# Kernel optimization log

Measured on AMD Instinct MI355X. Metric: run time of the kernel, lower is better.

Reference implementation:

```python
import jax, jax.numpy as jnp
import numpy as np
import math

B, N, D = 8, 4096, 1024
H = 8          # num_heads
NC = 2         # n_classes


def setup_inputs() -> dict:
    key = jax.random.key(0)
    ks = jax.random.split(key, 12)
    s = 1.0 / math.sqrt(D)
    return {
        "inputs": jax.random.normal(ks[0], (B, N, D), jnp.float32),
        # enc: Linear(D, 1) + Sigmoid
        "W_enc": jax.random.normal(ks[1], (1, D), jnp.float32) * s,
        "b_enc": jnp.zeros((1,), jnp.float32),
        "cls_token": jax.random.normal(ks[2], (1, 1, D), jnp.float32) * s,
        # depthwise Conv2d(D, D, 3, padding=1, groups=D)
        "conv_w": jax.random.normal(ks[3], (D, 1, 3, 3), jnp.float32) * 0.1,
        "conv_b": jnp.zeros((D,), jnp.float32),
        # MAB projections (torch Linear weight layout [out, in])
        "Wq": jax.random.normal(ks[4], (D, D), jnp.float32) * s,
        "bq": jnp.zeros((D,), jnp.float32),
        "Wk": jax.random.normal(ks[5], (D, D), jnp.float32) * s,
        "bk": jnp.zeros((D,), jnp.float32),
        "Wv": jax.random.normal(ks[6], (D, D), jnp.float32) * s,
        "bv": jnp.zeros((D,), jnp.float32),
        "Wo": jax.random.normal(ks[7], (D, D), jnp.float32) * s,
        "bo": jnp.zeros((D,), jnp.float32),
        # final classifier Linear(D, NC)
        "Wfc": jax.random.normal(ks[8], (NC, D), jnp.float32) * s,
        "bfc": jnp.zeros((NC,), jnp.float32),
    }


def reference(inputs, W_enc, b_enc, cls_token, conv_w, conv_b,
              Wq, bq, Wk, bk, Wv, bv, Wo, bo, Wfc, bfc):
    b, n, d = inputs.shape
    # ---- recalib(option='max', k=1): top-1 instance per bag as query ----
    a1 = jax.nn.sigmoid(inputs @ W_enc.T + b_enc)[..., 0]            # [B, N]
    idx = jnp.argmax(a1, axis=1)                                      # [B]
    Q = jnp.take_along_axis(inputs, idx[:, None, None], axis=1)       # [B, 1, D]
    # ---- shift_feature ----
    inputs = jax.nn.relu(inputs - Q)
    # ---- pad to square grid, prepend cls token ----
    _H = int(np.ceil(np.sqrt(n)))
    add = _H * _H - n
    x = jnp.concatenate([inputs, inputs[:, :add, :]], axis=1)         # [B, _H*_H, D]
    cls = jnp.broadcast_to(cls_token, (b, 1, d))
    x = jnp.concatenate([cls, x], axis=1)                             # [B, S, D]
    cls_tok, feat = x[:, 0], x[:, 1:]
    # ---- depthwise conv residual on the 2D grid ----
    cnn = feat.transpose(0, 2, 1).reshape(b, d, _H, _H)               # [B, C, H, W]
    conv = jax.lax.conv_general_dilated(
        cnn, conv_w, window_strides=(1, 1), padding='SAME',
        dimension_numbers=('NCHW', 'OIHW', 'NCHW'),
        feature_group_count=d) + conv_b[None, :, None, None]
    cnn = conv + cnn
    xf = cnn.reshape(b, d, _H * _H).transpose(0, 2, 1)
    x = jnp.concatenate([cls_tok[:, None, :], xf], axis=1)            # [B, S, D]
    # ---- MAB(Q, x): manual multi-head attention ----
    Qp = Q @ Wq.T + bq                                                # [B, 1, D]
    K = x @ Wk.T + bk                                                 # [B, S, D]
    V = x @ Wv.T + bv
    dh = d // H
    qh = Qp.reshape(b, 1, H, dh).transpose(0, 2, 1, 3)                # [B, H, 1, dh]
    kh = K.reshape(b, -1, H, dh).transpose(0, 2, 1, 3)                # [B, H, S, dh]
    vh = V.reshape(b, -1, H, dh).transpose(0, 2, 1, 3)
    # NOTE: original scales by sqrt(dim_V), not sqrt(d_head)
    logits = jnp.einsum('bhqd,bhkd->bhqk', qh, kh) / jnp.asarray(math.sqrt(d), jnp.float32)
    A = jax.nn.softmax(logits, axis=-1)
    oh = qh + jnp.einsum('bhqk,bhkd->bhqd', A, vh)                    # residual inside heads
    O = oh.transpose(0, 2, 1, 3).reshape(b, 1, d)                     # [B, 1, D]
    O = O + jax.nn.relu(O @ Wo.T + bo)
    bag = O[:, 0]                                                     # [B, D]
    out = bag @ Wfc.T + bfc                                           # [B, NC]
    return out
```

## Files before the change

kernel.cpp:

```cpp
#include <hip/hip_runtime.h>
#include <hip/hip_bf16.h>


#define NTOK 4096
#define DD 1024

#define FO_ARG 0
#define FO_S1  16
#define FO_CWT 4160
#define FO_QP  13376
#define FO_W   21568
#define FO_MS  87232
#define FO_YP  95424
#define FO_Y   4289728
#define FO_O1  4355264
#define FO_O2  4363456

#define LSTRIDE 101

__global__ void k_init(const float* __restrict__ convw, float* __restrict__ cwT) {
  int gid = blockIdx.x * 256 + threadIdx.x;
  if (gid < 9216) {
    int d = gid / 9, p = gid - d * 9;
    cwT[p * DD + d] = convw[gid];
  }
}

__global__ void k_argmax1(const float* __restrict__ inp, const float* __restrict__ Wenc,
                          const float* __restrict__ benc, unsigned long long* __restrict__ s1buf) {
  __shared__ unsigned long long lb[4];
  int wave = threadIdx.x >> 6, lane = threadIdx.x & 63;
  int b = blockIdx.x >> 8;
  int r0 = ((blockIdx.x & 255) << 4) + (wave << 2);
  const float4* base = (const float4*)(inp + ((size_t)b * NTOK + r0) * DD);
  const float4* wp = (const float4*)Wenc;
  float s0 = 0.f, s1 = 0.f, s2 = 0.f, s3 = 0.f;
#pragma unroll
  for (int k = 0; k < 4; ++k) {
    int off = lane + (k << 6);
    float4 w4 = wp[off];
    float4 a0 = base[off];
    float4 a1 = base[256 + off];
    float4 a2 = base[512 + off];
    float4 a3 = base[768 + off];
    s0 = fmaf(w4.x, a0.x, s0); s0 = fmaf(w4.y, a0.y, s0); s0 = fmaf(w4.z, a0.z, s0); s0 = fmaf(w4.w, a0.w, s0);
    s1 = fmaf(w4.x, a1.x, s1); s1 = fmaf(w4.y, a1.y, s1); s1 = fmaf(w4.z, a1.z, s1); s1 = fmaf(w4.w, a1.w, s1);
    s2 = fmaf(w4.x, a2.x, s2); s2 = fmaf(w4.y, a2.y, s2); s2 = fmaf(w4.z, a2.z, s2); s2 = fmaf(w4.w, a2.w, s2);
    s3 = fmaf(w4.x, a3.x, s3); s3 = fmaf(w4.y, a3.y, s3); s3 = fmaf(w4.z, a3.z, s3); s3 = fmaf(w4.w, a3.w, s3);
  }
#pragma unroll
  for (int mk = 32; mk >= 1; mk >>= 1) {
    s0 += __shfl_xor(s0, mk); s1 += __shfl_xor(s1, mk);
    s2 += __shfl_xor(s2, mk); s3 += __shfl_xor(s3, mk);
  }
  if (lane == 0) {
    float be = benc[0];
    float v[4] = {s0 + be, s1 + be, s2 + be, s3 + be};
    unsigned long long bst = 0ull;
#pragma unroll
    for (int i = 0; i < 4; ++i) {
      unsigned u = __float_as_uint(v[i]);
      u = (u & 0x80000000u) ? ~u : (u | 0x80000000u);
      unsigned long long p = ((unsigned long long)u << 32) |
                             (unsigned long long)(0xFFFFFFFFu - (unsigned)(r0 + i));
      bst = bst > p ? bst : p;
    }
    lb[wave] = bst;
  }
  __syncthreads();
  if (threadIdx.x == 0) {
    unsigned long long m = lb[0];
#pragma unroll
    for (int i = 1; i < 4; ++i) m = m > lb[i] ? m : lb[i];
    s1buf[blockIdx.x] = m;
  }
}

__global__ void k_argmax2(const unsigned long long* __restrict__ s1buf,
                          unsigned long long* __restrict__ argbest) {
  __shared__ unsigned long long red[256];
  int tid = threadIdx.x, b = blockIdx.x;
  red[tid] = s1buf[b * 256 + tid];
  __syncthreads();
  for (int s = 128; s > 0; s >>= 1) {
    if (tid < s) { unsigned long long o = red[tid + s]; if (o > red[tid]) red[tid] = o; }
    __syncthreads();
  }
  if (tid == 0) argbest[b] = red[0];
}

__global__ void k_qp(const float* __restrict__ inp, const float* __restrict__ Wq,
                     const float* __restrict__ bq, const unsigned long long* __restrict__ argbest,
                     float* __restrict__ Qp) {
  int wave = threadIdx.x >> 6, lane = threadIdx.x & 63;
  int b = blockIdx.x >> 8;
  int i = ((blockIdx.x & 255) << 2) + wave;
  unsigned idx = 0xFFFFFFFFu - (unsigned)(argbest[b] & 0xFFFFFFFFull);
  const float4* qr = (const float4*)(inp + ((size_t)b * NTOK + idx) * DD);
  const float4* wr = (const float4*)(Wq + (size_t)i * DD);
  float s = 0.f;
#pragma unroll
  for (int k = 0; k < 4; ++k) {
    float4 a = wr[lane + (k << 6)], x = qr[lane + (k << 6)];
    s = fmaf(a.x, x.x, s); s = fmaf(a.y, x.y, s);
    s = fmaf(a.z, x.z, s); s = fmaf(a.w, x.w, s);
  }
  for (int m = 32; m > 0; m >>= 1) s += __shfl_xor(s, m);
  if (lane == 0) Qp[b * DD + i] = s + bq[i];
}

__global__ void k_w(const float* __restrict__ Wk, const float* __restrict__ Qp,
                    float* __restrict__ wbuf) {
  __shared__ float qs[1024];
  __shared__ float sred[2048];
  const int tid = threadIdx.x;
  const int h = blockIdx.x >> 5, jb = blockIdx.x & 31;
  {
    int b = tid >> 5, i4 = tid & 31;
    ((float4*)qs)[b * 32 + i4] = ((const float4*)Qp)[b * 256 + (h << 5) + i4];
  }
  __syncthreads();
  const int jl = tid & 31, ig = tid >> 5;
  const float* wkp = Wk + (size_t)((h << 7) + (ig << 4)) * DD + (jb << 5) + jl;
  float acc[8];
#pragma unroll
  for (int b = 0; b < 8; ++b) acc[b] = 0.f;
#pragma unroll
  for (int ii = 0; ii < 16; ++ii) {
    float wv = wkp[(size_t)ii * DD];
    int i = (ig << 4) + ii;
#pragma unroll
    for (int b = 0; b < 8; ++b) acc[b] = fmaf(qs[(b << 7) + i], wv, acc[b]);
  }
#pragma unroll
  for (int b = 0; b < 8; ++b) sred[ig * 256 + (b << 5) + jl] = acc[b];
  __syncthreads();
  {
    int b = tid >> 5, j2 = tid & 31;
    float s = 0.f;
#pragma unroll
    for (int g = 0; g < 8; ++g) s += sred[g * 256 + (b << 5) + j2];
    wbuf[(size_t)((b << 3) + h) * DD + (jb << 5) + j2] = s;
  }
}

__global__ __launch_bounds__(512, 4) void k_fused(
    const float* __restrict__ inp, const float* __restrict__ convb,
    const float* __restrict__ cwT, const float* __restrict__ wbuf,
    const unsigned long long* __restrict__ argbest,
    float2* __restrict__ msbuf, float* __restrict__ ypart) {
  __shared__ float4 sred4[32 * LSTRIDE];
  __shared__ float atile[512];
  const int tid = threadIdx.x, bx = blockIdx.x;
  const int b = bx >> 6, tile = bx & 63;
  const int R0 = (tile >> 3) << 3, C0 = (tile & 7) << 3;
  const unsigned idxq = 0xFFFFFFFFu - (unsigned)(argbest[b] & 0xFFFFFFFFull);
  const float* inpb = inp + (size_t)b * NTOK * DD;
  const float* qrow = inpb + (size_t)idxq * DD;
  const int gg = tid & 31, ts = tid >> 5;
  const int jg = tid >> 5, rq = (tid >> 3) & 3, ca = tid & 7;
  const int r0a = rq << 1;

  float acc[2][8];
#pragma unroll
  for (int i = 0; i < 2; ++i)
#pragma unroll
    for (int h = 0; h < 8; ++h) acc[i][h] = 0.f;

  for (int cidx = 0; cidx < 8; ++cidx) {
    const int jc = cidx << 7;
    __syncthreads();
    {
      const int js = jc + (gg << 2);
      float4 qv = *(const float4*)(qrow + js);
      for (int t = ts; t < 100; t += 16) {
        int tr = t / 10, tc = t - tr * 10;
        int gr = R0 - 1 + tr, gc = C0 - 1 + tc;
        float4 v = make_float4(0.f, 0.f, 0.f, 0.f);
        if (gr >= 0 && gr < 64 && gc >= 0 && gc < 64) {
          float4 rv = *(const float4*)(inpb + (size_t)((gr << 6) + gc) * DD + js);
          v.x = fmaxf(rv.x - qv.x, 0.f); v.y = fmaxf(rv.y - qv.y, 0.f);
          v.z = fmaxf(rv.z - qv.z, 0.f); v.w = fmaxf(rv.w - qv.w, 0.f);
        }
        sred4[gg * LSTRIDE + t] = v;
      }
    }
    __syncthreads();
#pragma unroll
    for (int sub = 0; sub < 2; ++sub) {
      const int g = (sub << 4) + jg;
      const int j4 = jc + (g << 2);
      float4 cwr[9];
#pragma unroll
      for (int p = 0; p < 9; ++p) cwr[p] = *(const float4*)(cwT + p * DD + j4);
      float4 cb4 = *(const float4*)(convb + j4);
      const float4* fb = sred4 + g * LSTRIDE;
      float4 x0 = cb4, x1 = cb4;
      {
        float4 rw[4][3];
#pragma unroll
        for (int rr = 0; rr < 4; ++rr)
#pragma unroll
          for (int dc = 0; dc < 3; ++dc)
            rw[rr][dc] = fb[(r0a + rr) * 10 + ca + dc];
#pragma unroll
        for (int dr = 0; dr < 3; ++dr)
#pragma unroll
          for (int dc = 0; dc < 3; ++dc) {
            float4 w = cwr[dr * 3 + dc];
            float4 f0 = rw[dr][dc], f1 = rw[dr + 1][dc];
            x0.x = fmaf(w.x, f0.x, x0.x); x0.y = fmaf(w.y, f0.y, x0.y);
            x0.z = fmaf(w.z, f0.z, x0.z); x0.w = fmaf(w.w, f0.w, x0.w);
            x1.x = fmaf(w.x, f1.x, x1.x); x1.y = fmaf(w.y, f1.y, x1.y);
            x1.z = fmaf(w.z, f1.z, x1.z); x1.w = fmaf(w.w, f1.w, x1.w);
          }
        x0.x += rw[1][1].x; x0.y += rw[1][1].y; x0.z += rw[1][1].z; x0.w += rw[1][1].w;
        x1.x += rw[2][1].x; x1.y += rw[2][1].y; x1.z += rw[2][1].z; x1.w += rw[2][1].w;
      }
#pragma unroll
      for (int h = 0; h < 8; ++h) {
        float4 whv = *(const float4*)(wbuf + (size_t)(b * 8 + h) * DD + j4);
        float a0 = acc[0][h], a1 = acc[1][h];
        a0 = fmaf(whv.x, x0.x, a0); a0 = fmaf(whv.y, x0.y, a0);
        a0 = fmaf(whv.z, x0.z, a0); a0 = fmaf(whv.w, x0.w, a0);
        a1 = fmaf(whv.x, x1.x, a1); a1 = fmaf(whv.y, x1.y, a1);
        a1 = fmaf(whv.z, x1.z, a1); a1 = fmaf(whv.w, x1.w, a1);
        acc[0][h] = a0; acc[1][h] = a1;
      }
    }
  }
  __syncthreads();
  float* red = (float*)sred4;
#pragma unroll
  for (int it = 0; it < 2; ++it)
#pragma unroll
    for (int h = 0; h < 8; ++h)
      red[jg * 512 + ((r0a + it) * 8 + ca) * 8 + h] = acc[it][h];
  __syncthreads();
  {
    int o = tid;
    float s = 0.f;
#pragma unroll
    for (int g = 0; g < 16; ++g) s += red[g * 512 + o];
    int h = o & 7, tok = o >> 3;
    atile[h * 64 + tok] = s * 0.03125f;
  }
  __syncthreads();
  if (tid < 256) {
    int hh = tid >> 5, sl = tid & 31;
    float l1 = atile[hh * 64 + sl], l2 = atile[hh * 64 + 32 + sl];
    float mx = fmaxf(l1, l2);
#pragma unroll
    for (int mk = 16; mk >= 1; mk >>= 1) mx = fmaxf(mx, __shfl_xor(mx, mk));
    float e1 = __expf(l1 - mx), e2 = __expf(l2 - mx);
    float Ssum = e1 + e2;
#pragma unroll
    for (int mk = 16; mk >= 1; mk >>= 1) Ssum += __shfl_xor(Ssum, mk);
    atile[hh * 64 + sl] = e1; atile[hh * 64 + 32 + sl] = e2;
    if (sl == 0) msbuf[(b * 8 + hh) * 64 + tile] = make_float2(mx, Ssum);
  }
  const int gB = tid >> 4, rh = (tid >> 3) & 1, cB = tid & 7;
  const int rbase = rh << 2;
  for (int cidx = 0; cidx < 8; ++cidx) {
    const int jc = cidx << 7;
    __syncthreads();
    {
      const int js = jc + (gg << 2);
      float4 qv = *(const float4*)(qrow + js);
      for (int t = ts; t < 100; t += 16) {
        int tr = t / 10, tc = t - tr * 10;
        int gr = R0 - 1 + tr, gc = C0 - 1 + tc;
        float4 v = make_float4(0.f, 0.f, 0.f, 0.f);
        if (gr >= 0 && gr < 64 && gc >= 0 && gc < 64) {
          float4 rv = *(const float4*)(inpb + (size_t)((gr << 6) + gc) * DD + js);
          v.x = fmaxf(rv.x - qv.x, 0.f); v.y = fmaxf(rv.y - qv.y, 0.f);
          v.z = fmaxf(rv.z - qv.z, 0.f); v.w = fmaxf(rv.w - qv.w, 0.f);
        }
        sred4[gg * LSTRIDE + t] = v;
      }
    }
    __syncthreads();
    const int j4 = jc + (gB << 2);
    float4 cwr[9];
#pragma unroll
    for (int p = 0; p < 9; ++p) cwr[p] = *(const float4*)(cwT + p * DD + j4);
    float4 cb4 = *(const float4*)(convb + j4);
    const float4* fb = sred4 + gB * LSTRIDE;
    float4 y4[8];
#pragma unroll
    for (int h = 0; h < 8; ++h) y4[h] = make_float4(0.f, 0.f, 0.f, 0.f);
    float4 w0[3], w1[3], w2[3];
#pragma unroll
    for (int dc = 0; dc < 3; ++dc) {
      w0[dc] = fb[rbase * 10 + cB + dc];
      w1[dc] = fb[(rbase + 1) * 10 + cB + dc];
    }
#pragma unroll
    for (int k = 0; k < 4; ++k) {
#pragma unroll
      for (int dc = 0; dc < 3; ++dc) w2[dc] = fb[(rbase + k + 2) * 10 + cB + dc];
      float4 x4 = cb4;
#pragma unroll
      for (int dc = 0; dc < 3; ++dc) {
        float4 wa = cwr[dc], wb = cwr[3 + dc], wc = cwr[6 + dc];
        x4.x = fmaf(wa.x, w0[dc].x, x4.x); x4.y = fmaf(wa.y, w0[dc].y, x4.y);
        x4.z = fmaf(wa.z, w0[dc].z, x4.z); x4.w = fmaf(wa.w, w0[dc].w, x4.w);
        x4.x = fmaf(wb.x, w1[dc].x, x4.x); x4.y = fmaf(wb.y, w1[dc].y, x4.y);
        x4.z = fmaf(wb.z, w1[dc].z, x4.z); x4.w = fmaf(wb.w, w1[dc].w, x4.w);
        x4.x = fmaf(wc.x, w2[dc].x, x4.x); x4.y = fmaf(wc.y, w2[dc].y, x4.y);
        x4.z = fmaf(wc.z, w2[dc].z, x4.z); x4.w = fmaf(wc.w, w2[dc].w, x4.w);
      }
      x4.x += w1[1].x; x4.y += w1[1].y; x4.z += w1[1].z; x4.w += w1[1].w;
      int tok = ((rbase + k) << 3) + cB;
#pragma unroll
      for (int h = 0; h < 8; ++h) {
        float a = atile[h * 64 + tok];
        y4[h].x = fmaf(a, x4.x, y4[h].x); y4[h].y = fmaf(a, x4.y, y4[h].y);
        y4[h].z = fmaf(a, x4.z, y4[h].z); y4[h].w = fmaf(a, x4.w, y4[h].w);
      }
#pragma unroll
      for (int dc = 0; dc < 3; ++dc) { w0[dc] = w1[dc]; w1[dc] = w2[dc]; }
    }
#pragma unroll
    for (int h = 0; h < 8; ++h)
#pragma unroll
      for (int mk = 8; mk >= 1; mk >>= 1) {
        y4[h].x += __shfl_xor(y4[h].x, mk);
        y4[h].y += __shfl_xor(y4[h].y, mk);
        y4[h].z += __shfl_xor(y4[h].z, mk);
        y4[h].w += __shfl_xor(y4[h].w, mk);
      }
    if ((tid & 15) == 0) {
#pragma unroll
      for (int h = 0; h < 8; ++h)
        *(float4*)(ypart + ((size_t)(b * 8 + h) * 64 + tile) * DD + j4) = y4[h];
    }
  }
}

__global__ void k_comb(const float2* __restrict__ msbuf, const float* __restrict__ wbuf,
                       const float* __restrict__ cls, const float* __restrict__ ypart,
                       float* __restrict__ ybuf) {
  __shared__ float redl[256];
  __shared__ float wgt[64];
  __shared__ float wclss;
  __shared__ float4 sacc[256];
  int tid = threadIdx.x;
  int bh = blockIdx.x >> 3, cs = blockIdx.x & 7;
  {
    float4 a = ((const float4*)(wbuf + (size_t)bh * DD))[tid];
    float4 c = ((const float4*)cls)[tid];
    redl[tid] = a.x * c.x + a.y * c.y + a.z * c.z + a.w * c.w;
  }
  __syncthreads();
  for (int s = 128; s > 0; s >>= 1) { if (tid < s) redl[tid] += redl[tid + s]; __syncthreads(); }
  float l0 = redl[0] * 0.03125f;
  if (tid < 64) {
    float2 ms = msbuf[bh * 64 + tid];
    float m = ms.x, S = ms.y;
    float M = m;
#pragma unroll
    for (int mk = 32; mk >= 1; mk >>= 1) M = fmaxf(M, __shfl_xor(M, mk));
    M = fmaxf(M, l0);
    float w = __expf(m - M);
    float z = S * w;
#pragma unroll
    for (int mk = 32; mk >= 1; mk >>= 1) z += __shfl_xor(z, mk);
    float ec = __expf(l0 - M);
    float Z = z + ec;
    wgt[tid] = w / Z;
    if (tid == 0) wclss = ec / Z;
  }
  __syncthreads();
  int ch4 = (cs << 5) + (tid & 31);
  int tg = tid >> 5;
  const float* yp = ypart + (size_t)bh * 64 * DD + (ch4 << 2);
  float4 acc = make_float4(0.f, 0.f, 0.f, 0.f);
#pragma unroll
  for (int tt = 0; tt < 8; ++tt) {
    int t = tg * 8 + tt;
    float w = wgt[t];
    float4 v = *(const float4*)(yp + (size_t)t * DD);
    acc.x = fmaf(w, v.x, acc.x); acc.y = fmaf(w, v.y, acc.y);
    acc.z = fmaf(w, v.z, acc.z); acc.w = fmaf(w, v.w, acc.w);
  }
  sacc[tg * 32 + (tid & 31)] = acc;
  __syncthreads();
  if (tid < 32) {
    int c4 = (cs << 5) + tid;
    float4 s = sacc[tid];
#pragma unroll
    for (int g = 1; g < 8; ++g) {
      float4 v = sacc[g * 32 + tid];
      s.x += v.x; s.y += v.y; s.z += v.z; s.w += v.w;
    }
    float wc = wclss;
    float4 cv = *(const float4*)(cls + (c4 << 2));
    s.x = fmaf(wc, cv.x, s.x); s.y = fmaf(wc, cv.y, s.y);
    s.z = fmaf(wc, cv.z, s.z); s.w = fmaf(wc, cv.w, s.w);
    *(float4*)(ybuf + (size_t)bh * DD + (c4 << 2)) = s;
  }
}

__global__ void k_o1(const float* __restrict__ Wv, const float* __restrict__ bv,
                     const float* __restrict__ Qp, const float* __restrict__ ybuf,
                     float* __restrict__ O1) {
  int wave = threadIdx.x >> 6, lane = threadIdx.x & 63;
  int b = blockIdx.x >> 8;
  int i = ((blockIdx.x & 255) << 2) + wave;
  int h = i >> 7;
  const float4* wr = (const float4*)(Wv + (size_t)i * DD);
  const float4* yr = (const float4*)(ybuf + (size_t)(b * 8 + h) * DD);
  float s = 0.f;
#pragma unroll
  for (int k = 0; k < 4; ++k) {
    float4 a = wr[lane + (k << 6)], x = yr[lane + (k << 6)];
    s = fmaf(a.x, x.x, s); s = fmaf(a.y, x.y, s);
    s = fmaf(a.z, x.z, s); s = fmaf(a.w, x.w, s);
  }
  for (int m = 32; m > 0; m >>= 1) s += __shfl_xor(s, m);
  if (lane == 0) O1[b * DD + i] = Qp[b * DD + i] + bv[i] + s;
}

__global__ void k_o2(const float* __restrict__ Wo, const float* __restrict__ bo,
                     const float* __restrict__ O1, float* __restrict__ O2) {
  int wave = threadIdx.x >> 6, lane = threadIdx.x & 63;
  int b = blockIdx.x >> 8;
  int i = ((blockIdx.x & 255) << 2) + wave;
  const float4* wr = (const float4*)(Wo + (size_t)i * DD);
  const float4* xr = (const float4*)(O1 + (size_t)b * DD);
  float s = 0.f;
#pragma unroll
  for (int k = 0; k < 4; ++k) {
    float4 a = wr[lane + (k << 6)], x = xr[lane + (k << 6)];
    s = fmaf(a.x, x.x, s); s = fmaf(a.y, x.y, s);
    s = fmaf(a.z, x.z, s); s = fmaf(a.w, x.w, s);
  }
  for (int m = 32; m > 0; m >>= 1) s += __shfl_xor(s, m);
  if (lane == 0) O2[b * DD + i] = O1[b * DD + i] + fmaxf(s + bo[i], 0.f);
}

__global__ void k_out(const float* __restrict__ Wfc, const float* __restrict__ bfc,
                      const float* __restrict__ O2, float* __restrict__ out) {
  int wave = threadIdx.x >> 6, lane = threadIdx.x & 63;
  for (int p = wave; p < 16; p += 4) {
    int b = p >> 1, cc = p & 1;
    const float4* o = (const float4*)(O2 + (size_t)b * DD);
    const float4* wr = (const float4*)(Wfc + (size_t)cc * DD);
    float s = 0.f;
#pragma unroll
    for (int k = 0; k < 4; ++k) {
      float4 a = o[lane + (k << 6)], x = wr[lane + (k << 6)];
      s = fmaf(a.x, x.x, s); s = fmaf(a.y, x.y, s);
      s = fmaf(a.z, x.z, s); s = fmaf(a.w, x.w, s);
    }
    for (int m = 32; m > 0; m >>= 1) s += __shfl_xor(s, m);
    if (lane == 0) out[p] = s + bfc[cc];
  }
}

extern "C" void kernel_launch(void* const* d_in, const int* in_sizes, int n_in,
                              void* d_out, int out_size, void* d_ws, size_t ws_size,
                              hipStream_t stream) {
  const float* inp   = (const float*)d_in[0];
  const float* Wenc  = (const float*)d_in[1];
  const float* benc  = (const float*)d_in[2];
  const float* cls   = (const float*)d_in[3];
  const float* convw = (const float*)d_in[4];
  const float* convb = (const float*)d_in[5];
  const float* Wq    = (const float*)d_in[6];
  const float* bq    = (const float*)d_in[7];
  const float* Wk    = (const float*)d_in[8];
  const float* bv    = (const float*)d_in[11];
  const float* Wv    = (const float*)d_in[10];
  const float* Wo    = (const float*)d_in[12];
  const float* bo    = (const float*)d_in[13];
  const float* Wfc   = (const float*)d_in[14];
  const float* bfc   = (const float*)d_in[15];
  float* out = (float*)d_out;
  float* W = (float*)d_ws;
  unsigned long long* argbest = (unsigned long long*)(W + FO_ARG);
  unsigned long long* s1buf   = (unsigned long long*)(W + FO_S1);
  float* cwT   = W + FO_CWT;
  float* Qp    = W + FO_QP;
  float* wbuf  = W + FO_W;
  float2* msbuf = (float2*)(W + FO_MS);
  float* ypart = W + FO_YP;
  float* ybuf  = W + FO_Y;
  float* O1    = W + FO_O1;
  float* O2    = W + FO_O2;

  hipLaunchKernelGGL(k_init,    dim3(36),   dim3(256), 0, stream, convw, cwT);
  hipLaunchKernelGGL(k_argmax1, dim3(2048), dim3(256), 0, stream, inp, Wenc, benc, s1buf);
  hipLaunchKernelGGL(k_argmax2, dim3(8),    dim3(256), 0, stream, s1buf, argbest);
  hipLaunchKernelGGL(k_qp,      dim3(2048), dim3(256), 0, stream, inp, Wq, bq, argbest, Qp);
  hipLaunchKernelGGL(k_w,       dim3(256),  dim3(256), 0, stream, Wk, Qp, wbuf);
  hipLaunchKernelGGL(k_fused,   dim3(512),  dim3(512), 0, stream, inp, convb, cwT, wbuf, argbest, msbuf, ypart);
  hipLaunchKernelGGL(k_comb,    dim3(512),  dim3(256), 0, stream, msbuf, wbuf, cls, ypart, ybuf);
  hipLaunchKernelGGL(k_o1,      dim3(2048), dim3(256), 0, stream, Wv, bv, Qp, ybuf, O1);
  hipLaunchKernelGGL(k_o2,      dim3(2048), dim3(256), 0, stream, Wo, bo, O1, O2);
  hipLaunchKernelGGL(k_out,     dim3(1),    dim3(256), 0, stream, Wfc, bfc, O2, out);
}
```

Baseline: 387.3 us.

## Split fused conv-attention kernel into channel-parallel logits, softmax and accumulate kernels

The single fused kernel ran 512 blocks, and each block looped over 8 channel chunks in two passes. It is replaced by three kernels. k_logits computes per-chunk partial logits over 4096 blocks. k_sm reduces those partials across chunks and does the tile-local softmax. k_yacc recomputes the conv and accumulates the weighted values, also over 4096 blocks with one chunk each. The goal is to fill the GPU far better than 512 large blocks could. The cost is two extra launches and an 8 MB partial-logit buffer round trip, stored in the ypart region. The per-block halo is still loaded twice per tile, as before.

```diff
diff --git a/kernel.cpp b/kernel.cpp
--- a/kernel.cpp
+++ b/kernel.cpp
@@ -15,6 +15,7 @@
 #define FO_Y   4289728
 #define FO_O1  4355264
 #define FO_O2  4363456
+#define FO_AW  4371648
 
 #define LSTRIDE 101
 
@@ -144,15 +145,14 @@
   }
 }
 
-__global__ __launch_bounds__(512, 4) void k_fused(
+__global__ __launch_bounds__(512, 6) void k_logits(
     const float* __restrict__ inp, const float* __restrict__ convb,
     const float* __restrict__ cwT, const float* __restrict__ wbuf,
     const unsigned long long* __restrict__ argbest,
-    float2* __restrict__ msbuf, float* __restrict__ ypart) {
+    float* __restrict__ plog) {
   __shared__ float4 sred4[32 * LSTRIDE];
-  __shared__ float atile[512];
   const int tid = threadIdx.x, bx = blockIdx.x;
-  const int b = bx >> 6, tile = bx & 63;
+  const int b = bx >> 9, tile = (bx >> 3) & 63, cidx = bx & 7;
   const int R0 = (tile >> 3) << 3, C0 = (tile & 7) << 3;
   const unsigned idxq = 0xFFFFFFFFu - (unsigned)(argbest[b] & 0xFFFFFFFFull);
   const float* inpb = inp + (size_t)b * NTOK * DD;
@@ -160,6 +160,7 @@
   const int gg = tid & 31, ts = tid >> 5;
   const int jg = tid >> 5, rq = (tid >> 3) & 3, ca = tid & 7;
   const int r0a = rq << 1;
+  const int jc = cidx << 7;
 
   float acc[2][8];
 #pragma unroll
@@ -167,66 +168,62 @@
 #pragma unroll
     for (int h = 0; h < 8; ++h) acc[i][h] = 0.f;
 
-  for (int cidx = 0; cidx < 8; ++cidx) {
-    const int jc = cidx << 7;
-    __syncthreads();
+  {
+    const int js = jc + (gg << 2);
+    float4 qv = *(const float4*)(qrow + js);
+    for (int t = ts; t < 100; t += 16) {
+      int tr = t / 10, tc = t - tr * 10;
+      int gr = R0 - 1 + tr, gc = C0 - 1 + tc;
+      float4 v = make_float4(0.f, 0.f, 0.f, 0.f);
+      if (gr >= 0 && gr < 64 && gc >= 0 && gc < 64) {
+        float4 rv = *(const float4*)(inpb + (size_t)((gr << 6) + gc) * DD + js);
+        v.x = fmaxf(rv.x - qv.x, 0.f); v.y = fmaxf(rv.y - qv.y, 0.f);
+        v.z = fmaxf(rv.z - qv.z, 0.f); v.w = fmaxf(rv.w - qv.w, 0.f);
+      }
+      sred4[gg * LSTRIDE + t] = v;
+    }
+  }
+  __syncthreads();
+#pragma unroll
+  for (int sub = 0; sub < 2; ++sub) {
+    const int g = (sub << 4) + jg;
+    const int j4 = jc + (g << 2);
+    float4 cwr[9];
+#pragma unroll
+    for (int p = 0; p < 9; ++p) cwr[p] = *(const float4*)(cwT + p * DD + j4);
+    float4 cb4 = *(const float4*)(convb + j4);
+    const float4* fb = sred4 + g * LSTRIDE;
+    float4 x0 = cb4, x1 = cb4;
     {
-      const int js = jc + (gg << 2);
-      float4 qv = *(const float4*)(qrow + js);
-      for (int t = ts; t < 100; t += 16) {
-        int tr = t / 10, tc = t - tr * 10;
-        int gr = R0 - 1 + tr, gc = C0 - 1 + tc;
-        float4 v = make_float4(0.f, 0.f, 0.f, 0.f);
-        if (gr >= 0 && gr < 64 && gc >= 0 && gc < 64) {
-          float4 rv = *(const float4*)(inpb + (size_t)((gr << 6) + gc) * DD + js);
-          v.x = fmaxf(rv.x - qv.x, 0.f); v.y = fmaxf(rv.y - qv.y, 0.f);
-          v.z = fmaxf(rv.z - qv.z, 0.f); v.w = fmaxf(rv.w - qv.w, 0.f);
+      float4 rw[4][3];
+#pragma unroll
+      for (int rr = 0; rr < 4; ++rr)
+#pragma unroll
+        for (int dc = 0; dc < 3; ++dc)
+          rw[rr][dc] = fb[(r0a + rr) * 10 + ca + dc];
+#pragma unroll
+      for (int dr = 0; dr < 3; ++dr)
+#pragma unroll
+        for (int dc = 0; dc < 3; ++dc) {
+          float4 w = cwr[dr * 3 + dc];
+          float4 f0 = rw[dr][dc], f1 = rw[dr + 1][dc];
+          x0.x = fmaf(w.x, f0.x, x0.x); x0.y = fmaf(w.y, f0.y, x0.y);
+          x0.z = fmaf(w.z, f0.z, x0.z); x0.w = fmaf(w.w, f0.w, x0.w);
+          x1.x = fmaf(w.x, f1.x, x1.x); x1.y = fmaf(w.y, f1.y, x1.y);
+          x1.z = fmaf(w.z, f1.z, x1.z); x1.w = fmaf(w.w, f1.w, x1.w);
         }
-        sred4[gg * LSTRIDE + t] = v;
-      }
-    }
-    __syncthreads();
-#pragma unroll
-    for (int sub = 0; sub < 2; ++sub) {
-      const int g = (sub << 4) + jg;
-      const int j4 = jc + (g << 2);
-      float4 cwr[9];
-#pragma unroll
-      for (int p = 0; p < 9; ++p) cwr[p] = *(const float4*)(cwT + p * DD + j4);
-      float4 cb4 = *(const float4*)(convb + j4);
-      const float4* fb = sred4 + g * LSTRIDE;
-      float4 x0 = cb4, x1 = cb4;
-      {
-        float4 rw[4][3];
-#pragma unroll
-        for (int rr = 0; rr < 4; ++rr)
-#pragma unroll
-          for (int dc = 0; dc < 3; ++dc)
-            rw[rr][dc] = fb[(r0a + rr) * 10 + ca + dc];
-#pragma unroll
-        for (int dr = 0; dr < 3; ++dr)
-#pragma unroll
-          for (int dc = 0; dc < 3; ++dc) {
-            float4 w = cwr[dr * 3 + dc];
-            float4 f0 = rw[dr][dc], f1 = rw[dr + 1][dc];
-            x0.x = fmaf(w.x, f0.x, x0.x); x0.y = fmaf(w.y, f0.y, x0.y);
-            x0.z = fmaf(w.z, f0.z, x0.z); x0.w = fmaf(w.w, f0.w, x0.w);
-            x1.x = fmaf(w.x, f1.x, x1.x); x1.y = fmaf(w.y, f1.y, x1.y);
-            x1.z = fmaf(w.z, f1.z, x1.z); x1.w = fmaf(w.w, f1.w, x1.w);
-          }
-        x0.x += rw[1][1].x; x0.y += rw[1][1].y; x0.z += rw[1][1].z; x0.w += rw[1][1].w;
-        x1.x += rw[2][1].x; x1.y += rw[2][1].y; x1.z += rw[2][1].z; x1.w += rw[2][1].w;
-      }
-#pragma unroll
-      for (int h = 0; h < 8; ++h) {
-        float4 whv = *(const float4*)(wbuf + (size_t)(b * 8 + h) * DD + j4);
-        float a0 = acc[0][h], a1 = acc[1][h];
-        a0 = fmaf(whv.x, x0.x, a0); a0 = fmaf(whv.y, x0.y, a0);
-        a0 = fmaf(whv.z, x0.z, a0); a0 = fmaf(whv.w, x0.w, a0);
-        a1 = fmaf(whv.x, x1.x, a1); a1 = fmaf(whv.y, x1.y, a1);
-        a1 = fmaf(whv.z, x1.z, a1); a1 = fmaf(whv.w, x1.w, a1);
-        acc[0][h] = a0; acc[1][h] = a1;
-      }
+      x0.x += rw[1][1].x; x0.y += rw[1][1].y; x0.z += rw[1][1].z; x0.w += rw[1][1].w;
+      x1.x += rw[2][1].x; x1.y += rw[2][1].y; x1.z += rw[2][1].z; x1.w += rw[2][1].w;
+    }
+#pragma unroll
+    for (int h = 0; h < 8; ++h) {
+      float4 whv = *(const float4*)(wbuf + (size_t)(b * 8 + h) * DD + j4);
+      float a0 = acc[0][h], a1 = acc[1][h];
+      a0 = fmaf(whv.x, x0.x, a0); a0 = fmaf(whv.y, x0.y, a0);
+      a0 = fmaf(whv.z, x0.z, a0); a0 = fmaf(whv.w, x0.w, a0);
+      a1 = fmaf(whv.x, x1.x, a1); a1 = fmaf(whv.y, x1.y, a1);
+      a1 = fmaf(whv.z, x1.z, a1); a1 = fmaf(whv.w, x1.w, a1);
+      acc[0][h] = a0; acc[1][h] = a1;
     }
   }
   __syncthreads();
@@ -238,103 +235,137 @@
       red[jg * 512 + ((r0a + it) * 8 + ca) * 8 + h] = acc[it][h];
   __syncthreads();
   {
-    int o = tid;
     float s = 0.f;
 #pragma unroll
-    for (int g = 0; g < 16; ++g) s += red[g * 512 + o];
-    int h = o & 7, tok = o >> 3;
-    atile[h * 64 + tok] = s * 0.03125f;
-  }
-  __syncthreads();
-  if (tid < 256) {
-    int hh = tid >> 5, sl = tid & 31;
-    float l1 = atile[hh * 64 + sl], l2 = atile[hh * 64 + 32 + sl];
-    float mx = fmaxf(l1, l2);
-#pragma unroll
-    for (int mk = 16; mk >= 1; mk >>= 1) mx = fmaxf(mx, __shfl_xor(mx, mk));
-    float e1 = __expf(l1 - mx), e2 = __expf(l2 - mx);
-    float Ssum = e1 + e2;
-#pragma unroll
-    for (int mk = 16; mk >= 1; mk >>= 1) Ssum += __shfl_xor(Ssum, mk);
-    atile[hh * 64 + sl] = e1; atile[hh * 64 + 32 + sl] = e2;
-    if (sl == 0) msbuf[(b * 8 + hh) * 64 + tile] = make_float2(mx, Ssum);
-  }
+    for (int g = 0; g < 16; ++g) s += red[g * 512 + tid];
+    plog[(size_t)bx * 512 + tid] = s;
+  }
+}
+
+__global__ void k_sm(const float* __restrict__ plog, float* __restrict__ aw,
+                     float2* __restrict__ msbuf) {
+  __shared__ float atile[512];
+  const int tid = threadIdx.x, bt = blockIdx.x;
+  const float* pp = plog + (size_t)bt * 8 * 512;
+  float s0 = 0.f, s1 = 0.f;
+#pragma unroll
+  for (int c = 0; c < 8; ++c) {
+    s0 += pp[c * 512 + tid];
+    s1 += pp[c * 512 + 256 + tid];
+  }
+  {
+    int o = tid, h = o & 7, tok = o >> 3;
+    atile[h * 64 + tok] = s0 * 0.03125f;
+    o = tid + 256; h = o & 7; tok = o >> 3;
+    atile[h * 64 + tok] = s1 * 0.03125f;
+  }
+  __syncthreads();
+  const int hh = tid >> 5, sl = tid & 31;
+  float l1 = atile[hh * 64 + sl], l2 = atile[hh * 64 + 32 + sl];
+  float mx = fmaxf(l1, l2);
+#pragma unroll
+  for (int mk = 16; mk >= 1; mk >>= 1) mx = fmaxf(mx, __shfl_xor(mx, mk));
+  float e1 = __expf(l1 - mx), e2 = __expf(l2 - mx);
+  float Ssum = e1 + e2;
+#pragma unroll
+  for (int mk = 16; mk >= 1; mk >>= 1) Ssum += __shfl_xor(Ssum, mk);
+  aw[(size_t)bt * 512 + hh * 64 + sl] = e1;
+  aw[(size_t)bt * 512 + hh * 64 + 32 + sl] = e2;
+  if (sl == 0) {
+    int b = bt >> 6, tile = bt & 63;
+    msbuf[((b << 3) + hh) * 64 + tile] = make_float2(mx, Ssum);
+  }
+}
+
+__global__ __launch_bounds__(512, 6) void k_yacc(
+    const float* __restrict__ inp, const float* __restrict__ convb,
+    const float* __restrict__ cwT, const float* __restrict__ aw,
+    const unsigned long long* __restrict__ argbest,
+    float* __restrict__ ypart) {
+  __shared__ float4 sred4[32 * LSTRIDE];
+  __shared__ float atile[512];
+  const int tid = threadIdx.x, bx = blockIdx.x;
+  const int b = bx >> 9, tile = (bx >> 3) & 63, cidx = bx & 7;
+  const int R0 = (tile >> 3) << 3, C0 = (tile & 7) << 3;
+  const unsigned idxq = 0xFFFFFFFFu - (unsigned)(argbest[b] & 0xFFFFFFFFull);
+  const float* inpb = inp + (size_t)b * NTOK * DD;
+  const float* qrow = inpb + (size_t)idxq * DD;
+  const int gg = tid & 31, ts = tid >> 5;
+  const int jc = cidx << 7;
+
+  atile[tid] = aw[(size_t)((b << 6) + tile) * 512 + tid];
+  {
+    const int js = jc + (gg << 2);
+    float4 qv = *(const float4*)(qrow + js);
+    for (int t = ts; t < 100; t += 16) {
+      int tr = t / 10, tc = t - tr * 10;
+      int gr = R0 - 1 + tr, gc = C0 - 1 + tc;
+      float4 v = make_float4(0.f, 0.f, 0.f, 0.f);
+      if (gr >= 0 && gr < 64 && gc >= 0 && gc < 64) {
+        float4 rv = *(const float4*)(inpb + (size_t)((gr << 6) + gc) * DD + js);
+        v.x = fmaxf(rv.x - qv.x, 0.f); v.y = fmaxf(rv.y - qv.y, 0.f);
+        v.z = fmaxf(rv.z - qv.z, 0.f); v.w = fmaxf(rv.w - qv.w, 0.f);
+      }
+      sred4[gg * LSTRIDE + t] = v;
+    }
+  }
+  __syncthreads();
   const int gB = tid >> 4, rh = (tid >> 3) & 1, cB = tid & 7;
   const int rbase = rh << 2;
-  for (int cidx = 0; cidx < 8; ++cidx) {
-    const int jc = cidx << 7;
-    __syncthreads();
-    {
-      const int js = jc + (gg << 2);
-      float4 qv = *(const float4*)(qrow + js);
-      for (int t = ts; t < 100; t += 16) {
-        int tr = t / 10, tc = t - tr * 10;
-        int gr = R0 - 1 + tr, gc = C0 - 1 + tc;
-        float4 v = make_float4(0.f, 0.f, 0.f, 0.f);
-        if (gr >= 0 && gr < 64 && gc >= 0 && gc < 64) {
-          float4 rv = *(const float4*)(inpb + (size_t)((gr << 6) + gc) * DD + js);
-          v.x = fmaxf(rv.x - qv.x, 0.f); v.y = fmaxf(rv.y - qv.y, 0.f);
-          v.z = fmaxf(rv.z - qv.z, 0.f); v.w = fmaxf(rv.w - qv.w, 0.f);
-        }
-        sred4[gg * LSTRIDE + t] = v;
-      }
-    }
-    __syncthreads();
-    const int j4 = jc + (gB << 2);
-    float4 cwr[9];
-#pragma unroll
-    for (int p = 0; p < 9; ++p) cwr[p] = *(const float4*)(cwT + p * DD + j4);
-    float4 cb4 = *(const float4*)(convb + j4);
-    const float4* fb = sred4 + gB * LSTRIDE;
-    float4 y4[8];
-#pragma unroll
-    for (int h = 0; h < 8; ++h) y4[h] = make_float4(0.f, 0.f, 0.f, 0.f);
-    float4 w0[3], w1[3], w2[3];
+  const int j4 = jc + (gB << 2);
+  float4 cwr[9];
+#pragma unroll
+  for (int p = 0; p < 9; ++p) cwr[p] = *(const float4*)(cwT + p * DD + j4);
+  float4 cb4 = *(const float4*)(convb + j4);
+  const float4* fb = sred4 + gB * LSTRIDE;
+  float4 y4[8];
+#pragma unroll
+  for (int h = 0; h < 8; ++h) y4[h] = make_float4(0.f, 0.f, 0.f, 0.f);
+  float4 w0[3], w1[3], w2[3];
+#pragma unroll
+  for (int dc = 0; dc < 3; ++dc) {
+    w0[dc] = fb[rbase * 10 + cB + dc];
+    w1[dc] = fb[(rbase + 1) * 10 + cB + dc];
+  }
+#pragma unroll
+  for (int k = 0; k < 4; ++k) {
+#pragma unroll
+    for (int dc = 0; dc < 3; ++dc) w2[dc] = fb[(rbase + k + 2) * 10 + cB + dc];
+    float4 x4 = cb4;
 #pragma unroll
     for (int dc = 0; dc < 3; ++dc) {
-      w0[dc] = fb[rbase * 10 + cB + dc];
-      w1[dc] = fb[(rbase + 1) * 10 + cB + dc];
-    }
-#pragma unroll
-    for (int k = 0; k < 4; ++k) {
-#pragma unroll
-      for (int dc = 0; dc < 3; ++dc) w2[dc] = fb[(rbase + k + 2) * 10 + cB + dc];
-      float4 x4 = cb4;
-#pragma unroll
-      for (int dc = 0; dc < 3; ++dc) {
-        float4 wa = cwr[dc], wb = cwr[3 + dc], wc = cwr[6 + dc];
-        x4.x = fmaf(wa.x, w0[dc].x, x4.x); x4.y = fmaf(wa.y, w0[dc].y, x4.y);
-        x4.z = fmaf(wa.z, w0[dc].z, x4.z); x4.w = fmaf(wa.w, w0[dc].w, x4.w);
-        x4.x = fmaf(wb.x, w1[dc].x, x4.x); x4.y = fmaf(wb.y, w1[dc].y, x4.y);
-        x4.z = fmaf(wb.z, w1[dc].z, x4.z); x4.w = fmaf(wb.w, w1[dc].w, x4.w);
-        x4.x = fmaf(wc.x, w2[dc].x, x4.x); x4.y = fmaf(wc.y, w2[dc].y, x4.y);
-        x4.z = fmaf(wc.z, w2[dc].z, x4.z); x4.w = fmaf(wc.w, w2[dc].w, x4.w);
-      }
-      x4.x += w1[1].x; x4.y += w1[1].y; x4.z += w1[1].z; x4.w += w1[1].w;
-      int tok = ((rbase + k) << 3) + cB;
-#pragma unroll
-      for (int h = 0; h < 8; ++h) {
-        float a = atile[h * 64 + tok];
-        y4[h].x = fmaf(a, x4.x, y4[h].x); y4[h].y = fmaf(a, x4.y, y4[h].y);
-        y4[h].z = fmaf(a, x4.z, y4[h].z); y4[h].w = fmaf(a, x4.w, y4[h].w);
-      }
-#pragma unroll
-      for (int dc = 0; dc < 3; ++dc) { w0[dc] = w1[dc]; w1[dc] = w2[dc]; }
-    }
+      float4 wa = cwr[dc], wb = cwr[3 + dc], wc = cwr[6 + dc];
+      x4.x = fmaf(wa.x, w0[dc].x, x4.x); x4.y = fmaf(wa.y, w0[dc].y, x4.y);
+      x4.z = fmaf(wa.z, w0[dc].z, x4.z); x4.w = fmaf(wa.w, w0[dc].w, x4.w);
+      x4.x = fmaf(wb.x, w1[dc].x, x4.x); x4.y = fmaf(wb.y, w1[dc].y, x4.y);
+      x4.z = fmaf(wb.z, w1[dc].z, x4.z); x4.w = fmaf(wb.w, w1[dc].w, x4.w);
+      x4.x = fmaf(wc.x, w2[dc].x, x4.x); x4.y = fmaf(wc.y, w2[dc].y, x4.y);
+      x4.z = fmaf(wc.z, w2[dc].z, x4.z); x4.w = fmaf(wc.w, w2[dc].w, x4.w);
+    }
+    x4.x += w1[1].x; x4.y += w1[1].y; x4.z += w1[1].z; x4.w += w1[1].w;
+    int tok = ((rbase + k) << 3) + cB;
+#pragma unroll
+    for (int h = 0; h < 8; ++h) {
+      float a = atile[h * 64 + tok];
+      y4[h].x = fmaf(a, x4.x, y4[h].x); y4[h].y = fmaf(a, x4.y, y4[h].y);
+      y4[h].z = fmaf(a, x4.z, y4[h].z); y4[h].w = fmaf(a, x4.w, y4[h].w);
+    }
+#pragma unroll
+    for (int dc = 0; dc < 3; ++dc) { w0[dc] = w1[dc]; w1[dc] = w2[dc]; }
+  }
+#pragma unroll
+  for (int h = 0; h < 8; ++h)
+#pragma unroll
+    for (int mk = 8; mk >= 1; mk >>= 1) {
+      y4[h].x += __shfl_xor(y4[h].x, mk);
+      y4[h].y += __shfl_xor(y4[h].y, mk);
+      y4[h].z += __shfl_xor(y4[h].z, mk);
+      y4[h].w += __shfl_xor(y4[h].w, mk);
+    }
+  if ((tid & 15) == 0) {
 #pragma unroll
     for (int h = 0; h < 8; ++h)
-#pragma unroll
-      for (int mk = 8; mk >= 1; mk >>= 1) {
-        y4[h].x += __shfl_xor(y4[h].x, mk);
-        y4[h].y += __shfl_xor(y4[h].y, mk);
-        y4[h].z += __shfl_xor(y4[h].z, mk);
-        y4[h].w += __shfl_xor(y4[h].w, mk);
-      }
-    if ((tid & 15) == 0) {
-#pragma unroll
-      for (int h = 0; h < 8; ++h)
-        *(float4*)(ypart + ((size_t)(b * 8 + h) * 64 + tile) * DD + j4) = y4[h];
-    }
+      *(float4*)(ypart + ((size_t)(b * 8 + h) * 64 + tile) * DD + j4) = y4[h];
   }
 }
 
@@ -486,6 +517,8 @@
   float* wbuf  = W + FO_W;
   float2* msbuf = (float2*)(W + FO_MS);
   float* ypart = W + FO_YP;
+  float* plog  = W + FO_YP;
+  float* aw    = W + FO_AW;
   float* ybuf  = W + FO_Y;
   float* O1    = W + FO_O1;
   float* O2    = W + FO_O2;
@@ -495,7 +528,9 @@
   hipLaunchKernelGGL(k_argmax2, dim3(8),    dim3(256), 0, stream, s1buf, argbest);
   hipLaunchKernelGGL(k_qp,      dim3(2048), dim3(256), 0, stream, inp, Wq, bq, argbest, Qp);
   hipLaunchKernelGGL(k_w,       dim3(256),  dim3(256), 0, stream, Wk, Qp, wbuf);
-  hipLaunchKernelGGL(k_fused,   dim3(512),  dim3(512), 0, stream, inp, convb, cwT, wbuf, argbest, msbuf, ypart);
+  hipLaunchKernelGGL(k_logits,  dim3(4096), dim3(512), 0, stream, inp, convb, cwT, wbuf, argbest, plog);
+  hipLaunchKernelGGL(k_sm,      dim3(512),  dim3(256), 0, stream, plog, aw, msbuf);
+  hipLaunchKernelGGL(k_yacc,    dim3(4096), dim3(512), 0, stream, inp, convb, cwT, aw, argbest, ypart);
   hipLaunchKernelGGL(k_comb,    dim3(512),  dim3(256), 0, stream, msbuf, wbuf, cls, ypart, ybuf);
   hipLaunchKernelGGL(k_o1,      dim3(2048), dim3(256), 0, stream, Wv, bv, Qp, ybuf, O1);
   hipLaunchKernelGGL(k_o2,      dim3(2048), dim3(256), 0, stream, Wo, bo, O1, O2);
```

New measurement: 455.4 us. 17.6% more time.
